# Performance work log

Hardware: AMD Instinct MI355X
Metric: run time of the kernel (lower is better)

The kernel has to match this reference:

```python
import jax, jax.numpy as jnp
import numpy as np

NUM_CLASSES = 80
STRIDES = (8, 16, 32)
FEATS = ((80, 80), (40, 40), (20, 20))
RADIUS = 2.5
CAND_K = 10


def make_grids():
    grids, strides = [], []
    for (h, w), s in zip(FEATS, STRIDES):
        gx, gy = jnp.meshgrid(jnp.arange(w), jnp.arange(h))  # xy indexing: gx=col, gy=row
        g = jnp.stack([gx, gy], -1).reshape(-1, 2).astype(jnp.float32)
        grids.append(g)
        strides.append(jnp.full((h * w, 1), float(s), jnp.float32))
    return jnp.concatenate(grids, 0), jnp.concatenate(strides, 0)  # [A,2], [A,1]


def decode_level(p, s):
    # p: [B, 85, h, w] -> decoded [B, h*w, 85]; xy/wh decoded, conf/cls stay logits
    b, c, h, w = p.shape
    out = p.reshape(b, c, h * w).transpose(0, 2, 1)
    gx, gy = jnp.meshgrid(jnp.arange(w), jnp.arange(h))
    g = jnp.stack([gx, gy], -1).reshape(1, -1, 2).astype(p.dtype)
    xy = (out[..., :2] + g) * s
    wh = jnp.exp(out[..., 2:4]) * s
    return jnp.concatenate([xy, wh, out[..., 4:]], -1)


def pairwise_iou_cxcywh(a, b):
    # a: [G,4], b: [A,4] -> [G,A]
    tl = jnp.maximum(a[:, None, :2] - a[:, None, 2:] * 0.5, b[None, :, :2] - b[None, :, 2:] * 0.5)
    br = jnp.minimum(a[:, None, :2] + a[:, None, 2:] * 0.5, b[None, :, :2] + b[None, :, 2:] * 0.5)
    wh = jnp.clip(br - tl, 0.0)
    inter = wh[..., 0] * wh[..., 1]
    area_a = (a[:, 2] * a[:, 3])[:, None]
    area_b = (b[:, 2] * b[:, 3])[None, :]
    return inter / (area_a + area_b - inter + 1e-16)


def elem_iou_cxcywh(a, b):
    # a, b: [...,4] aligned -> [...]
    tl = jnp.maximum(a[..., :2] - a[..., 2:] * 0.5, b[..., :2] - b[..., 2:] * 0.5)
    br = jnp.minimum(a[..., :2] + a[..., 2:] * 0.5, b[..., :2] + b[..., 2:] * 0.5)
    wh = jnp.clip(br - tl, 0.0)
    inter = wh[..., 0] * wh[..., 1]
    area = a[..., 2] * a[..., 3] + b[..., 2] * b[..., 3]
    return inter / (area - inter + 1e-16)


def bce_logits(x, t):
    return jnp.maximum(x, 0.0) - x * t + jnp.log1p(jnp.exp(-jnp.abs(x)))


def assign_one(gt_b, gt_c, pbox, pconf, pcls, xy_center, stride_v):
    # SimOTA dynamic matching for one image. gt_b:[G,4], gt_c:[G], pbox:[A,4], pconf:[A,1], pcls:[A,C]
    G = gt_b.shape[0]
    # center-in-box / center-in-mirror(radius) masks
    bmin = gt_b[:, :2] - gt_b[:, 2:] * 0.5
    bmax = gt_b[:, :2] + gt_b[:, 2:] * 0.5
    d = jnp.concatenate([xy_center[None] - bmin[:, None], bmax[:, None] - xy_center[None]], -1)  # [G,A,4]
    in_box = jnp.min(d, -1) > 0.0
    mmin = gt_b[:, None, :2] - RADIUS * stride_v[None]
    mmax = gt_b[:, None, :2] + RADIUS * stride_v[None]
    d2 = jnp.concatenate([xy_center[None] - mmin, mmax - xy_center[None]], -1)
    in_mir = jnp.min(d2, -1) > 0.0
    union = jnp.any(in_box, 0) | jnp.any(in_mir, 0)  # [A]
    inter = in_box & in_mir  # [G,A]

    iou = pairwise_iou_cxcywh(gt_b, pbox)  # [G,A]
    iou_cost = -jnp.log(iou + 1e-8)
    # cls cost: BCE(sqrt(sigmoid(cls)*sigmoid(conf)), one_hot).sum(C), computed without [G,A,C]
    p = jnp.sqrt(jax.nn.sigmoid(pcls) * jax.nn.sigmoid(pconf))  # [A,C]
    logp = jnp.clip(jnp.log(jnp.clip(p, 1e-12)), -100.0)
    log1mp = jnp.clip(jnp.log(jnp.clip(1.0 - p, 1e-12)), -100.0)
    cls_cost = -(logp[:, gt_c].T - log1mp[:, gt_c].T + log1mp.sum(-1)[None, :])  # [G,A]

    cost = cls_cost + 3.0 * iou_cost + 1e5 * (~inter).astype(cost_dtype(pcls))
    cost = jnp.where(union[None, :], cost, 1e15)  # exclude anchors outside union (bool-index in torch)
    iou_m = jnp.where(union[None, :], iou, 0.0)

    # dynamic k per gt = clamp(int(sum top10 iou), 1)
    topk_iou, _ = jax.lax.top_k(iou_m, CAND_K)
    dyn_k = jnp.maximum(topk_iou.sum(1).astype(jnp.int32), 1)  # [G]
    _, idx = jax.lax.top_k(-cost, CAND_K)  # smallest-cost anchors per gt [G,10]
    valid = (jnp.arange(CAND_K)[None, :] < dyn_k[:, None]).astype(cost.dtype)
    mm = jnp.zeros_like(cost).at[jnp.arange(G)[:, None], idx].set(valid)  # [G,A]

    # resolve anchors matched to >1 gt by argmin cost
    multi = mm.sum(0) > 1.0
    best = jnp.argmin(cost, 0)  # [A]
    mm = jnp.where(multi[None, :], jax.nn.one_hot(best, G, dtype=mm.dtype).T, mm)

    fg = mm.sum(0) > 0.0  # [A]
    gt_idx = jnp.argmax(mm, 0)  # [A]
    match_iou = (mm * iou).sum(0)  # [A]
    return fg, gt_idx, match_iou


def cost_dtype(x):
    return x.dtype


def setup_inputs() -> dict:
    key = jax.random.key(0)
    ks = jax.random.split(key, 5)
    B, G = 32, 16
    p8 = jax.random.normal(ks[0], (B, 85, 80, 80), jnp.float32)
    p16 = jax.random.normal(ks[1], (B, 85, 40, 40), jnp.float32)
    p32 = jax.random.normal(ks[2], (B, 85, 20, 20), jnp.float32)
    u = jax.random.uniform(ks[3], (B, G, 4), jnp.float32)
    gt_boxes = jnp.concatenate([32.0 + u[..., :2] * 576.0, 16.0 + u[..., 2:] * 112.0], -1)
    gt_cls = jax.random.randint(ks[4], (B, G), 0, 80, dtype=jnp.int32)
    return {"p8": p8, "p16": p16, "p32": p32, "gt_boxes": gt_boxes, "gt_cls": gt_cls}


def reference(p8, p16, p32, gt_boxes, gt_cls):
    outs = [decode_level(p, s) for p, s in zip((p8, p16, p32), STRIDES)]
    outputs = jnp.concatenate(outs, 1)  # [B, 8400, 85]
    grids, stride_v = make_grids()
    xy_center = (grids + 0.5) * stride_v  # [A,2]
    pbox, pconf, pcls = outputs[..., :4], outputs[..., 4:5], outputs[..., 5:]

    sg = jax.lax.stop_gradient  # assignment is under torch.no_grad
    fg, gt_idx, match_iou = jax.vmap(assign_one, in_axes=(0, 0, 0, 0, 0, None, None))(
        gt_boxes, gt_cls, sg(pbox), sg(pconf), sg(pcls), xy_center, stride_v)
    match_iou = sg(match_iou)

    tgt_box = jnp.take_along_axis(gt_boxes, gt_idx[..., None], axis=1)  # [B,A,4]
    tgt_cls_id = jnp.take_along_axis(gt_cls, gt_idx, axis=1)  # [B,A]
    tgt_cls = jax.nn.one_hot(tgt_cls_id, NUM_CLASSES, dtype=outputs.dtype) * match_iou[..., None]
    fgf = fg.astype(outputs.dtype)

    iou_e = elem_iou_cxcywh(pbox, tgt_box)  # [B,A]
    loss_box = jnp.sum(fgf * (1.0 - iou_e ** 2))            # IOUloss, fg only
    loss_conf = jnp.sum(bce_logits(pconf[..., 0], fgf))     # all anchors
    loss_cls = jnp.sum(fgf[..., None] * bce_logits(pcls, tgt_cls))  # fg only
    n_fg = jnp.maximum(jnp.sum(fgf), 1.0)
    return (5.0 * loss_box + loss_conf + loss_cls) / n_fg
```

## Files before the change

### kernel.cpp

```cpp
#include <hip/hip_runtime.h>
#include <hip/hip_bf16.h>

#define A_TOT 8400
#define NB 32
#define NG 16
#define NC 80

#define K1_GX 132
#define NWAVE (K1_GX * NB * 4)

#define L2E 1.44269504088896340736f
#define LN2 0.69314718055994530942f

__device__ inline float fexp2(float x) { return __builtin_amdgcn_exp2f(x); }
__device__ inline float flog2(float x) { return __builtin_amdgcn_logf(x); }
__device__ inline float frcp(float x)  { return __builtin_amdgcn_rcpf(x); }
__device__ inline float fsqrtf_(float x) { return __builtin_amdgcn_sqrtf(x); }

__device__ inline float iou_cxcywh(float acx, float acy, float aw, float ah,
                                   float bcx, float bcy, float bw, float bh) {
    float tlx = fmaxf(acx - aw * 0.5f, bcx - bw * 0.5f);
    float tly = fmaxf(acy - ah * 0.5f, bcy - bh * 0.5f);
    float brx = fminf(acx + aw * 0.5f, bcx + bw * 0.5f);
    float bry = fminf(acy + ah * 0.5f, bcy + bh * 0.5f);
    float w = fmaxf(brx - tlx, 0.0f);
    float h = fmaxf(bry - tly, 0.0f);
    float inter = w * h;
    return inter / (aw * ah + bw * bh - inter + 1e-16f);
}

__device__ inline float dval_of(float x, float sc) {
    float u = fexp2(-x * L2E);
    float sx = frcp(1.0f + u);
    float pr = fsqrtf_(sx * sc);
    float lp  = fmaxf(LN2 * flog2(fmaxf(pr, 1e-12f)), -100.0f);
    float l1p = fmaxf(LN2 * flog2(fmaxf(1.0f - pr, 1e-12f)), -100.0f);
    return lp - l1p;
}

__device__ inline float cost_fast(float iou, float d, float sp, unsigned m, int g) {
    if (!((m >> 16) & 1u)) return 1e15f;
    float c = -(d + sp) - 3.0f * LN2 * flog2(iou + 1e-8f);
    if (!((m >> g) & 1u)) c += 100000.0f;
    return c;
}

__device__ inline unsigned long long umax64(unsigned long long a, unsigned long long b) {
    return a > b ? a : b;
}
__device__ inline unsigned long long umin64(unsigned long long a, unsigned long long b) {
    return a < b ? a : b;
}

__device__ inline const float* lvl_base(int a, int b, const float* p8, const float* p16,
                                        const float* p32, int& hw, int& HW, int& W, float& s) {
    if (a < 6400) { hw = a;        HW = 6400; W = 80; s = 8.0f;  return p8  + (size_t)b * 85 * 6400; }
    if (a < 8000) { hw = a - 6400; HW = 1600; W = 40; s = 16.0f; return p16 + (size_t)b * 85 * 1600; }
    { hw = a - 8000; HW = 400; W = 20; s = 32.0f; return p32 + (size_t)b * 85 * 400; }
}

__global__ void k0_zero(float* acc) {
    if (threadIdx.x < 8) acc[threadIdx.x] = 0.0f;
}

__global__ __launch_bounds__(256) void k1_decode(
    const float* __restrict__ p8, const float* __restrict__ p16, const float* __restrict__ p32,
    const float* __restrict__ gtb,
    float4* __restrict__ pbox, float* __restrict__ sl1p,
    float* __restrict__ s0cls, float* __restrict__ confw, float* __restrict__ ssc,
    unsigned* __restrict__ umask, float* __restrict__ part) {
    int b = blockIdx.y;
    int tid = threadIdx.x;
    int a = blockIdx.x * 64 + (tid >> 2);
    int quad = tid & 3;
    float bce0_conf = 0.0f;
    if (a < A_TOT) {
        int hw, HW, W;
        float s;
        const float* base = lvl_base(a, b, p8, p16, p32, hw, HW, W, s);

        float cf = base[4 * HW + hw];
        float uc = fexp2(-cf * L2E);
        float suc = 1.0f + uc;
        float sc = frcp(suc);

        const float* cbase = base + (5 + quad * 20) * HW + hw;
        float x[20];
#pragma unroll
        for (int j = 0; j < 20; j++) x[j] = cbase[j * HW];
        float s0 = 0.0f, suml1p = 0.0f;
#pragma unroll
        for (int j = 0; j < 20; j++) {
            float u = fexp2(-x[j] * L2E);
            float su = 1.0f + u;
            s0 += x[j] + LN2 * flog2(su);
            float pr = fsqrtf_(frcp(su) * sc);
            suml1p += fmaxf(LN2 * flog2(fmaxf(1.0f - pr, 1e-12f)), -100.0f);
        }
        s0 += __shfl_xor(s0, 1, 64);
        s0 += __shfl_xor(s0, 2, 64);
        suml1p += __shfl_xor(suml1p, 1, 64);
        suml1p += __shfl_xor(suml1p, 2, 64);

        if (quad == 0) {
            float tx = base[hw], ty = base[HW + hw];
            float tw = base[2 * HW + hw], th = base[3 * HW + hw];
            int gx = hw % W, gy = hw / W;
            float pcx = (tx + (float)gx) * s;
            float pcy = (ty + (float)gy) * s;
            float pw = fexp2(tw * L2E) * s;
            float ph = fexp2(th * L2E) * s;

            bce0_conf = cf + LN2 * flog2(suc);

            float xc = ((float)gx + 0.5f) * s;
            float yc = ((float)gy + 0.5f) * s;
            unsigned m = 0;
            bool uni = false;
            float r = 2.5f * s;
#pragma unroll 4
            for (int g = 0; g < NG; g++) {
                float gcx = gtb[(b * NG + g) * 4 + 0];
                float gcy = gtb[(b * NG + g) * 4 + 1];
                float gw  = gtb[(b * NG + g) * 4 + 2];
                float gh  = gtb[(b * NG + g) * 4 + 3];
                bool ib = (xc > gcx - gw * 0.5f) && (gcx + gw * 0.5f > xc) &&
                          (yc > gcy - gh * 0.5f) && (gcy + gh * 0.5f > yc);
                bool im = (xc > gcx - r) && (gcx + r > xc) &&
                          (yc > gcy - r) && (gcy + r > yc);
                uni |= (ib || im);
                if (ib && im) m |= (1u << g);
            }
            if (uni) m |= (1u << 16);

            size_t i = (size_t)b * A_TOT + a;
            pbox[i] = make_float4(pcx, pcy, pw, ph);
            confw[i] = cf;
            ssc[i] = sc;
            sl1p[i] = suml1p;
            s0cls[i] = s0;
            umask[i] = m;
        }
    }
    float v = bce0_conf;
    for (int off = 32; off; off >>= 1) v += __shfl_down(v, off, 64);
    if ((tid & 63) == 0) {
        int wave = (blockIdx.y * gridDim.x + blockIdx.x) * 4 + (tid >> 6);
        part[wave] = v;
    }
}

__global__ __launch_bounds__(256) void k2_assign(
    const float* __restrict__ gtb, const int* __restrict__ gtc,
    const float4* __restrict__ pbox, const float* __restrict__ sl1p,
    const float* __restrict__ ssc, const unsigned* __restrict__ umask,
    const float* __restrict__ p8, const float* __restrict__ p16, const float* __restrict__ p32,
    int* __restrict__ sel, int* __restrict__ nsel) {
    __shared__ unsigned long long wred[4];
    int blk = blockIdx.x;
    int b = blk >> 4, g = blk & 15;
    int tid = threadIdx.x;

    float gcx = gtb[blk * 4 + 0], gcy = gtb[blk * 4 + 1];
    float gw = gtb[blk * 4 + 2],  gh = gtb[blk * 4 + 3];
    int cg = gtc[blk];

    unsigned long long topI[10];
    unsigned long long topC[10];
#pragma unroll
    for (int i = 0; i < 10; i++) { topI[i] = 0ull; topC[i] = 0xFFFFFFFFFFFFFFFFull; }

    for (int a = tid; a < A_TOT; a += 256) {
        size_t i = (size_t)b * A_TOT + a;
        float4 pb = pbox[i];
        unsigned m = umask[i];
        float iou = iou_cxcywh(gcx, gcy, gw, gh, pb.x, pb.y, pb.z, pb.w);
        float mi = ((m >> 16) & 1u) ? iou : 0.0f;

        int hw, HW, W;
        float s;
        const float* base = lvl_base(a, b, p8, p16, p32, hw, HW, W, s);
        float x = base[(5 + cg) * HW + hw];
        float sc = ssc[i];
        float d = dval_of(x, sc);
        float sp = sl1p[i];
        float cost = cost_fast(iou, d, sp, m, g);

        if (mi > 0.0f) {
            unsigned long long kI = ((unsigned long long)__float_as_uint(mi) << 32) | (unsigned)a;
            if (kI > topI[9]) {
                unsigned long long v = kI;
#pragma unroll
                for (int i2 = 0; i2 < 10; i2++) {
                    unsigned long long big = umax64(topI[i2], v);
                    v = umin64(topI[i2], v);
                    topI[i2] = big;
                }
            }
        }
        unsigned long long kC = ((unsigned long long)__float_as_uint(cost) << 32) | (unsigned)a;
        if (kC < topC[9]) {
            unsigned long long v = kC;
#pragma unroll
            for (int i2 = 0; i2 < 10; i2++) {
                unsigned long long sml = umin64(topC[i2], v);
                v = umax64(topC[i2], v);
                topC[i2] = sml;
            }
        }
    }

    float ksum = 0.0f;
    for (int rr = 0; rr < 10; rr++) {
        unsigned long long h = topI[0];
        for (int off = 32; off; off >>= 1) h = umax64(h, __shfl_xor(h, off, 64));
        if ((tid & 63) == 0) wred[tid >> 6] = h;
        __syncthreads();
        unsigned long long w = umax64(umax64(wred[0], wred[1]), umax64(wred[2], wred[3]));
        ksum += __uint_as_float((unsigned)(w >> 32));
        if (topI[0] == w) {
#pragma unroll
            for (int i = 0; i < 9; i++) topI[i] = topI[i + 1];
            topI[9] = 0ull;
        }
        __syncthreads();
    }
    int dynk = (int)ksum;
    if (dynk < 1) dynk = 1;
    if (dynk > 10) dynk = 10;

    for (int rr = 0; rr < 10; rr++) {
        unsigned long long h = topC[0];
        for (int off = 32; off; off >>= 1) h = umin64(h, __shfl_xor(h, off, 64));
        if ((tid & 63) == 0) wred[tid >> 6] = h;
        __syncthreads();
        unsigned long long w = umin64(umin64(wred[0], wred[1]), umin64(wred[2], wred[3]));
        if (tid == 0) sel[blk * 10 + rr] = (int)(w & 0xffffffffu);
        if (topC[0] == w) {
#pragma unroll
            for (int i = 0; i < 9; i++) topC[i] = topC[i + 1];
            topC[9] = 0xFFFFFFFFFFFFFFFFull;
        }
        __syncthreads();
    }
    if (tid == 0) nsel[blk] = dynk;
}

__global__ __launch_bounds__(256) void k3_resolve(
    const float* __restrict__ gtb, const int* __restrict__ gtc,
    const float4* __restrict__ pbox, const float* __restrict__ sl1p,
    const unsigned* __restrict__ umask,
    const float* __restrict__ confw, const float* __restrict__ ssc,
    const float* __restrict__ s0cls,
    const int* __restrict__ sel, const int* __restrict__ nsel,
    const float* __restrict__ p8, const float* __restrict__ p16, const float* __restrict__ p32,
    float* __restrict__ acc) {
    __shared__ unsigned tag[A_TOT];
    __shared__ float gb[NG * 4];
    __shared__ int gc[NG];
    __shared__ float red[256];
    int b = blockIdx.x, tid = threadIdx.x;

    for (int a = tid; a < A_TOT; a += 256) tag[a] = 0;
    if (tid < NG * 4) gb[tid] = gtb[b * NG * 4 + tid];
    if (tid < NG) gc[tid] = gtc[b * NG + tid];
    __syncthreads();

    if (tid < NG * 10) {
        int g = tid / 10, k = tid % 10;
        if (k < nsel[b * NG + g]) {
            int a = sel[(b * NG + g) * 10 + k];
            atomicAdd(&tag[a], 0x10000u + (unsigned)(g + 1));
        }
    }
    __syncthreads();

    float lbox = 0.0f, lconfc = 0.0f, lcls = 0.0f, nfg = 0.0f;
    for (int a = tid; a < A_TOT; a += 256) {
        unsigned t = tag[a];
        unsigned cnt = t >> 16;
        if (!cnt) continue;
        size_t i = (size_t)b * A_TOT + a;
        float4 pb = pbox[i];
        int hw, HW, W;
        float s;
        const float* base = lvl_base(a, b, p8, p16, p32, hw, HW, W, s);
        int gs;
        if (cnt == 1) {
            gs = (int)(t & 0xffffu) - 1;
        } else {
            unsigned m = umask[i];
            float sp = sl1p[i];
            float sc = ssc[i];
            float bc = 3.402823466e38f;
            gs = 0;
            for (int g = 0; g < NG; g++) {
                float iou = iou_cxcywh(gb[g * 4], gb[g * 4 + 1], gb[g * 4 + 2], gb[g * 4 + 3],
                                       pb.x, pb.y, pb.z, pb.w);
                float x = base[(5 + gc[g]) * HW + hw];
                float d = dval_of(x, sc);
                float c = cost_fast(iou, d, sp, m, g);
                if (c < bc) { bc = c; gs = g; }
            }
        }
        float miou = iou_cxcywh(gb[gs * 4], gb[gs * 4 + 1], gb[gs * 4 + 2], gb[gs * 4 + 3],
                                pb.x, pb.y, pb.z, pb.w);
        int cid = gc[gs];
        float xcid = base[(5 + cid) * HW + hw];

        lbox += 1.0f - miou * miou;
        lconfc -= confw[i];
        lcls += s0cls[i] - xcid * miou;
        nfg += 1.0f;
    }

    float vals[4] = {lbox, lconfc, lcls, nfg};
    for (int i = 0; i < 4; i++) {
        red[tid] = vals[i];
        __syncthreads();
        for (int s2 = 128; s2 > 0; s2 >>= 1) {
            if (tid < s2) red[tid] += red[tid + s2];
            __syncthreads();
        }
        if (tid == 0) atomicAdd(&acc[1 + i], red[0]);
        __syncthreads();
    }
}

__global__ __launch_bounds__(256) void k4_final(
    const float* __restrict__ part, const float* __restrict__ acc, float* __restrict__ out) {
    __shared__ float red[256];
    int tid = threadIdx.x;
    float v = 0.0f;
    for (int i = tid; i < NWAVE; i += 256) v += part[i];
    red[tid] = v;
    __syncthreads();
    for (int s2 = 128; s2 > 0; s2 >>= 1) {
        if (tid < s2) red[tid] += red[tid + s2];
        __syncthreads();
    }
    if (tid == 0) {
        float nfg = acc[4];
        if (nfg < 1.0f) nfg = 1.0f;
        out[0] = (5.0f * acc[1] + (red[0] + acc[2]) + acc[3]) / nfg;
    }
}

extern "C" void kernel_launch(void* const* d_in, const int* in_sizes, int n_in,
                              void* d_out, int out_size, void* d_ws, size_t ws_size,
                              hipStream_t stream) {
    const float* p8  = (const float*)d_in[0];
    const float* p16 = (const float*)d_in[1];
    const float* p32 = (const float*)d_in[2];
    const float* gtb = (const float*)d_in[3];
    const int*   gtc = (const int*)d_in[4];

    char* w = (char*)d_ws;
    float4* pbox = (float4*)w;                 w += (size_t)NB * A_TOT * sizeof(float4);
    float* sl1p  = (float*)w;                  w += (size_t)NB * A_TOT * sizeof(float);
    float* s0c   = (float*)w;                  w += (size_t)NB * A_TOT * sizeof(float);
    float* conf  = (float*)w;                  w += (size_t)NB * A_TOT * sizeof(float);
    float* sscp  = (float*)w;                  w += (size_t)NB * A_TOT * sizeof(float);
    unsigned* um = (unsigned*)w;               w += (size_t)NB * A_TOT * sizeof(unsigned);
    int* sel     = (int*)w;                    w += (size_t)NB * NG * 10 * sizeof(int);
    int* nsel    = (int*)w;                    w += (size_t)NB * NG * sizeof(int);
    float* part  = (float*)w;                  w += (size_t)NWAVE * sizeof(float);
    float* acc   = (float*)w;

    k0_zero<<<1, 64, 0, stream>>>(acc);
    k1_decode<<<dim3(K1_GX, NB), 256, 0, stream>>>(
        p8, p16, p32, gtb, pbox, sl1p, s0c, conf, sscp, um, part);
    k2_assign<<<NB * NG, 256, 0, stream>>>(gtb, gtc, pbox, sl1p, sscp, um,
                                           p8, p16, p32, sel, nsel);
    k3_resolve<<<NB, 256, 0, stream>>>(gtb, gtc, pbox, sl1p, um, conf, sscp, s0c,
                                       sel, nsel, p8, p16, p32, acc);
    k4_final<<<1, 256, 0, stream>>>(part, acc, (float*)d_out);
}
```

Measured before the change: 209.0 us.

## Widen assignment blocks, split resolve across anchor chunks, drop atomic accumulators

The per-GT assignment kernel moves from 256 to 1024 threads per block, and its cross-wave reduction is widened to 16 waves. It now skips the class-logit gather and cost computation for anchors outside the center mask. The resolve kernel is split into 8 anchor chunks per image, using a smaller shared tag array, which gives 256 blocks instead of 32. Partial sums are written to a buffer and reduced in the final kernel, which removes the zeroing kernel and the atomics. The costs are more barrier rounds per selection step in the wider assignment blocks and a larger final reduction.

```diff
diff --git a/kernel.cpp b/kernel.cpp
--- a/kernel.cpp
+++ b/kernel.cpp
@@ -8,6 +8,8 @@
 
 #define K1_GX 132
 #define NWAVE (K1_GX * NB * 4)
+#define K3_CH 8
+#define K3_W  1050
 
 #define L2E 1.44269504088896340736f
 #define LN2 0.69314718055994530942f
@@ -57,10 +59,6 @@
     if (a < 6400) { hw = a;        HW = 6400; W = 80; s = 8.0f;  return p8  + (size_t)b * 85 * 6400; }
     if (a < 8000) { hw = a - 6400; HW = 1600; W = 40; s = 16.0f; return p16 + (size_t)b * 85 * 1600; }
     { hw = a - 8000; HW = 400; W = 20; s = 32.0f; return p32 + (size_t)b * 85 * 400; }
-}
-
-__global__ void k0_zero(float* acc) {
-    if (threadIdx.x < 8) acc[threadIdx.x] = 0.0f;
 }
 
 __global__ __launch_bounds__(256) void k1_decode(
@@ -150,13 +148,13 @@
     }
 }
 
-__global__ __launch_bounds__(256) void k2_assign(
+__global__ __launch_bounds__(1024, 8) void k2_assign(
     const float* __restrict__ gtb, const int* __restrict__ gtc,
     const float4* __restrict__ pbox, const float* __restrict__ sl1p,
     const float* __restrict__ ssc, const unsigned* __restrict__ umask,
     const float* __restrict__ p8, const float* __restrict__ p16, const float* __restrict__ p32,
     int* __restrict__ sel, int* __restrict__ nsel) {
-    __shared__ unsigned long long wred[4];
+    __shared__ unsigned long long wred[16];
     int blk = blockIdx.x;
     int b = blk >> 4, g = blk & 15;
     int tid = threadIdx.x;
@@ -170,21 +168,24 @@
 #pragma unroll
     for (int i = 0; i < 10; i++) { topI[i] = 0ull; topC[i] = 0xFFFFFFFFFFFFFFFFull; }
 
-    for (int a = tid; a < A_TOT; a += 256) {
+    for (int a = tid; a < A_TOT; a += 1024) {
         size_t i = (size_t)b * A_TOT + a;
         float4 pb = pbox[i];
         unsigned m = umask[i];
         float iou = iou_cxcywh(gcx, gcy, gw, gh, pb.x, pb.y, pb.z, pb.w);
-        float mi = ((m >> 16) & 1u) ? iou : 0.0f;
-
-        int hw, HW, W;
-        float s;
-        const float* base = lvl_base(a, b, p8, p16, p32, hw, HW, W, s);
-        float x = base[(5 + cg) * HW + hw];
-        float sc = ssc[i];
-        float d = dval_of(x, sc);
-        float sp = sl1p[i];
-        float cost = cost_fast(iou, d, sp, m, g);
+
+        float cost = 1e15f;
+        float mi = 0.0f;
+        if ((m >> 16) & 1u) {
+            mi = iou;
+            int hw, HW, W;
+            float s;
+            const float* base = lvl_base(a, b, p8, p16, p32, hw, HW, W, s);
+            float x = base[(5 + cg) * HW + hw];
+            float d = dval_of(x, ssc[i]);
+            cost = -(d + sl1p[i]) - 3.0f * LN2 * flog2(iou + 1e-8f);
+            if (!((m >> g) & 1u)) cost += 100000.0f;
+        }
 
         if (mi > 0.0f) {
             unsigned long long kI = ((unsigned long long)__float_as_uint(mi) << 32) | (unsigned)a;
@@ -216,7 +217,9 @@
         for (int off = 32; off; off >>= 1) h = umax64(h, __shfl_xor(h, off, 64));
         if ((tid & 63) == 0) wred[tid >> 6] = h;
         __syncthreads();
-        unsigned long long w = umax64(umax64(wred[0], wred[1]), umax64(wred[2], wred[3]));
+        unsigned long long w = wred[0];
+#pragma unroll
+        for (int j = 1; j < 16; j++) w = umax64(w, wred[j]);
         ksum += __uint_as_float((unsigned)(w >> 32));
         if (topI[0] == w) {
 #pragma unroll
@@ -234,7 +237,9 @@
         for (int off = 32; off; off >>= 1) h = umin64(h, __shfl_xor(h, off, 64));
         if ((tid & 63) == 0) wred[tid >> 6] = h;
         __syncthreads();
-        unsigned long long w = umin64(umin64(wred[0], wred[1]), umin64(wred[2], wred[3]));
+        unsigned long long w = wred[0];
+#pragma unroll
+        for (int j = 1; j < 16; j++) w = umin64(w, wred[j]);
         if (tid == 0) sel[blk * 10 + rr] = (int)(w & 0xffffffffu);
         if (topC[0] == w) {
 #pragma unroll
@@ -254,14 +259,15 @@
     const float* __restrict__ s0cls,
     const int* __restrict__ sel, const int* __restrict__ nsel,
     const float* __restrict__ p8, const float* __restrict__ p16, const float* __restrict__ p32,
-    float* __restrict__ acc) {
-    __shared__ unsigned tag[A_TOT];
+    float4* __restrict__ part3) {
+    __shared__ unsigned tag[K3_W];
     __shared__ float gb[NG * 4];
     __shared__ int gc[NG];
     __shared__ float red[256];
-    int b = blockIdx.x, tid = threadIdx.x;
-
-    for (int a = tid; a < A_TOT; a += 256) tag[a] = 0;
+    int b = blockIdx.y, chunk = blockIdx.x, tid = threadIdx.x;
+    int a0 = chunk * K3_W;
+
+    for (int j = tid; j < K3_W; j += 256) tag[j] = 0;
     if (tid < NG * 4) gb[tid] = gtb[b * NG * 4 + tid];
     if (tid < NG) gc[tid] = gtc[b * NG + tid];
     __syncthreads();
@@ -270,16 +276,18 @@
         int g = tid / 10, k = tid % 10;
         if (k < nsel[b * NG + g]) {
             int a = sel[(b * NG + g) * 10 + k];
-            atomicAdd(&tag[a], 0x10000u + (unsigned)(g + 1));
+            if (a >= a0 && a < a0 + K3_W)
+                atomicAdd(&tag[a - a0], 0x10000u + (unsigned)(g + 1));
         }
     }
     __syncthreads();
 
     float lbox = 0.0f, lconfc = 0.0f, lcls = 0.0f, nfg = 0.0f;
-    for (int a = tid; a < A_TOT; a += 256) {
-        unsigned t = tag[a];
+    for (int j = tid; j < K3_W; j += 256) {
+        unsigned t = tag[j];
         unsigned cnt = t >> 16;
         if (!cnt) continue;
+        int a = a0 + j;
         size_t i = (size_t)b * A_TOT + a;
         float4 pb = pbox[i];
         int hw, HW, W;
@@ -315,6 +323,7 @@
     }
 
     float vals[4] = {lbox, lconfc, lcls, nfg};
+    float outv[4];
     for (int i = 0; i < 4; i++) {
         red[tid] = vals[i];
         __syncthreads();
@@ -322,27 +331,36 @@
             if (tid < s2) red[tid] += red[tid + s2];
             __syncthreads();
         }
-        if (tid == 0) atomicAdd(&acc[1 + i], red[0]);
-        __syncthreads();
-    }
+        outv[i] = red[0];
+        __syncthreads();
+    }
+    if (tid == 0)
+        part3[blockIdx.y * K3_CH + chunk] = make_float4(outv[0], outv[1], outv[2], outv[3]);
 }
 
 __global__ __launch_bounds__(256) void k4_final(
-    const float* __restrict__ part, const float* __restrict__ acc, float* __restrict__ out) {
+    const float* __restrict__ part, const float4* __restrict__ part3, float* __restrict__ out) {
     __shared__ float red[256];
     int tid = threadIdx.x;
     float v = 0.0f;
     for (int i = tid; i < NWAVE; i += 256) v += part[i];
-    red[tid] = v;
-    __syncthreads();
-    for (int s2 = 128; s2 > 0; s2 >>= 1) {
-        if (tid < s2) red[tid] += red[tid + s2];
+    float4 p = part3[tid & 255];
+    float vals[5] = {v, p.x, p.y, p.z, p.w};
+    float tot[5];
+    for (int i = 0; i < 5; i++) {
+        red[tid] = vals[i];
+        __syncthreads();
+        for (int s2 = 128; s2 > 0; s2 >>= 1) {
+            if (tid < s2) red[tid] += red[tid + s2];
+            __syncthreads();
+        }
+        tot[i] = red[0];
         __syncthreads();
     }
     if (tid == 0) {
-        float nfg = acc[4];
+        float nfg = tot[4];
         if (nfg < 1.0f) nfg = 1.0f;
-        out[0] = (5.0f * acc[1] + (red[0] + acc[2]) + acc[3]) / nfg;
+        out[0] = (5.0f * tot[1] + (tot[0] + tot[2]) + tot[3]) / nfg;
     }
 }
 
@@ -365,14 +383,13 @@
     int* sel     = (int*)w;                    w += (size_t)NB * NG * 10 * sizeof(int);
     int* nsel    = (int*)w;                    w += (size_t)NB * NG * sizeof(int);
     float* part  = (float*)w;                  w += (size_t)NWAVE * sizeof(float);
-    float* acc   = (float*)w;
-
-    k0_zero<<<1, 64, 0, stream>>>(acc);
+    float4* part3 = (float4*)w;                w += (size_t)NB * K3_CH * sizeof(float4);
+
     k1_decode<<<dim3(K1_GX, NB), 256, 0, stream>>>(
         p8, p16, p32, gtb, pbox, sl1p, s0c, conf, sscp, um, part);
-    k2_assign<<<NB * NG, 256, 0, stream>>>(gtb, gtc, pbox, sl1p, sscp, um,
-                                           p8, p16, p32, sel, nsel);
-    k3_resolve<<<NB, 256, 0, stream>>>(gtb, gtc, pbox, sl1p, um, conf, sscp, s0c,
-                                       sel, nsel, p8, p16, p32, acc);
-    k4_final<<<1, 256, 0, stream>>>(part, acc, (float*)d_out);
-}
+    k2_assign<<<NB * NG, 1024, 0, stream>>>(gtb, gtc, pbox, sl1p, sscp, um,
+                                            p8, p16, p32, sel, nsel);
+    k3_resolve<<<dim3(K3_CH, NB), 256, 0, stream>>>(gtb, gtc, pbox, sl1p, um, conf, sscp, s0c,
+                                                    sel, nsel, p8, p16, p32, part3);
+    k4_final<<<1, 256, 0, stream>>>(part, part3, (float*)d_out);
+}
```

Result: slower. 260.0 us (+24.4%).
